# Kernel optimization log

Measured on AMD Instinct MI355X. Metric: run time of the kernel, lower is better.

Reference implementation:

```python
import jax, jax.numpy as jnp
import numpy as np

N, M, C, T, H, W = 32, 20, 512, 4, 7, 7  # batch, max_others, channels, t, h, w
L = 4  # temp_pos_len
STD = 0.01


def setup_inputs() -> dict:
    key = jax.random.key(0)
    ks = jax.random.split(key, 12)
    return {
        "person": jax.random.normal(ks[0], (N, C, T, H, W), jnp.float32),
        "others": jax.random.normal(ks[1], (N, M, C, T, H, W), jnp.float32),
        "Wq": jax.random.normal(ks[2], (C, C), jnp.float32) * STD,
        "bq": jax.random.normal(ks[3], (C,), jnp.float32) * STD,
        "Wk": jax.random.normal(ks[4], (C, C), jnp.float32) * STD,
        "bk": jax.random.normal(ks[5], (C,), jnp.float32) * STD,
        "Wv": jax.random.normal(ks[6], (C, C), jnp.float32) * STD,
        "bv": jax.random.normal(ks[7], (C,), jnp.float32) * STD,
        "Wo": jax.random.normal(ks[8], (C, C), jnp.float32) * STD,
        "bo": jax.random.normal(ks[9], (C,), jnp.float32) * STD,
        "pos_k": jax.random.normal(ks[10], (L, C), jnp.float32) * 0.02,
        "pos_v": jax.random.normal(ks[11], (L, C), jnp.float32) * 0.02,
    }


def reference(person, others, Wq, bq, Wk, bk, Wv, bv, Wo, bo, pos_k, pos_v):
    n, c, t, h, w = person.shape
    _, m, _, to, ho, wo = others.shape
    scale = c ** (-0.5)

    # 1x1x1 conv projections == channel matmuls
    q = jnp.einsum('oc,ncthw->nothw', Wq, person) + bq[None, :, None, None, None]
    k = jnp.einsum('oc,nmcthw->nmothw', Wk, others) + bk[None, None, :, None, None, None]
    v = jnp.einsum('oc,nmcthw->nmothw', Wv, others) + bv[None, None, :, None, None, None]

    # additive temporal positional bias on K/V: others split into L temporal groups
    Lp = pos_k.shape[0]
    P = m // Lp  # max_person_per_sec
    k = (k.reshape(n, Lp, P, c, to, ho, wo)
         + pos_k[None, :, None, :, None, None, None]).reshape(n, m, c, to, ho, wo)
    v = (v.reshape(n, Lp, P, c, to, ho, wo)
         + pos_v[None, :, None, :, None, None, None]).reshape(n, m, c, to, ho, wo)

    S = t * h * w          # query length
    K = m * to * ho * wo   # key length
    qf = q.reshape(n, c, S).transpose(0, 2, 1)                              # [n,S,c]
    kf = k.reshape(n, m, c, to * ho * wo).transpose(0, 1, 3, 2).reshape(n, K, c)
    vf = v.reshape(n, m, c, to * ho * wo).transpose(0, 1, 3, 2).reshape(n, K, c)

    attn = jax.nn.softmax(jnp.einsum('nsc,nkc->nsk', qf, kf) * scale, axis=-1)
    o = jnp.einsum('nsk,nkc->nsc', attn, vf)                                # [n,S,c]
    o = o.transpose(0, 2, 1).reshape(n, c, t, h, w)

    # LayerNorm over [c,t,h,w] per sample, no affine
    mu = jnp.mean(o, axis=(1, 2, 3, 4), keepdims=True)
    var = jnp.var(o, axis=(1, 2, 3, 4), keepdims=True)
    o = (o - mu) * jax.lax.rsqrt(var + 1e-5)

    o = jax.nn.relu(o)
    o = jnp.einsum('oc,ncthw->nothw', Wo, o) + bo[None, :, None, None, None]
    return o + person  # shortcut is identity (dim_person == dim_out)
```

## Files before the change

### kernel.cpp

```cpp
#include <hip/hip_runtime.h>
#include <hip/hip_bf16.h>

#define N_B 32
#define M_O 20
#define C_C 512
#define S_S 196
#define S_P 208
#define K_K 3920
#define K_P 4096
#define SCALEF 0.044194173824159216f

typedef short s4v __attribute__((ext_vector_type(4)));
typedef short s8v __attribute__((ext_vector_type(8)));
typedef float f4v __attribute__((ext_vector_type(4)));

__device__ __forceinline__ f4v mfma16(s8v a, s8v b, f4v c){
  return __builtin_amdgcn_mfma_f32_16x16x32_bf16(a, b, c, 0, 0, 0);
}
__device__ __forceinline__ unsigned short f2b(float x){
  __hip_bfloat16 h = __float2bfloat16(x);
  return *reinterpret_cast<unsigned short*>(&h);
}
__device__ __forceinline__ float b2f(short u){
  unsigned int v = ((unsigned int)(unsigned short)u) << 16;
  return __uint_as_float(v);
}

#define GLOAD16(g, l) __builtin_amdgcn_global_load_lds( \
    (const __attribute__((address_space(1))) unsigned int*)(g), \
    (__attribute__((address_space(3))) unsigned int*)(l), 16, 0, 0)

__global__ void k_sentinel(float* out, float v){ out[threadIdx.x] = v; }

__global__ void k_cvt(const float* __restrict__ w0, const float* __restrict__ w1,
                      const float* __restrict__ w2, const float* __restrict__ w3,
                      unsigned short* __restrict__ out){
  int i = blockIdx.x*256 + threadIdx.x;
  int m = i >> 16;
  int r = i & 65535;
  const float* s = (m==0)?w0:((m==1)?w1:((m==2)?w2:w3));
  f4v v = ((const f4v*)s)[r];
  s4v o = { (short)f2b(v[0]), (short)f2b(v[1]), (short)f2b(v[2]), (short)f2b(v[3]) };
  ((s4v*)out)[i] = o;
}

__global__ __launch_bounds__(256) void k_tr(const float* __restrict__ X,
                                            unsigned short* __restrict__ Xt){
  const int cc = blockIdx.x * 64;
  const int slab = blockIdx.y;
  const int tid = threadIdx.x;
  __shared__ unsigned short A[196][72];
  const int row = tid >> 2;
  const int j   = tid & 3;
  const float* src = X + (size_t)slab*(C_C*S_S) + (size_t)(cc+row)*S_S;
  for (int p = j; p < 49; p += 4){
    f4v v = *(const f4v*)(src + p*4);
    int s = p*4;
    A[s+0][row] = f2b(v[0]);
    A[s+1][row] = f2b(v[1]);
    A[s+2][row] = f2b(v[2]);
    A[s+3][row] = f2b(v[3]);
  }
  __syncthreads();
  unsigned short* dst = Xt + (size_t)slab*(S_S*C_C) + cc;
  for (int v = tid; v < S_S*8; v += 256){
    int s = v >> 3, c8 = v & 7;
    *(s8v*)(dst + (size_t)s*C_C + c8*8) = *(const s8v*)&A[s][c8*8];
  }
}

template<bool HASV>
__global__ __launch_bounds__(256, 2) void k_projgemm(
    const unsigned short* __restrict__ Xt,
    const unsigned short* __restrict__ W1, const float* __restrict__ b1, const float* __restrict__ pos1,
    const unsigned short* __restrict__ W2, const float* __restrict__ b2, const float* __restrict__ pos2,
    unsigned short* __restrict__ outK, unsigned short* __restrict__ outVT)
{
  const int id = blockIdx.x;
  const int work = HASV ? ((id & 7)*980 + (id >> 3)) : id;
  const int ct    = HASV ? (work & 3) : (work & 1);
  const int rtile = HASV ? (work >> 2) : (work >> 1);
  const int r0 = rtile*64;
  const int cb = ct * (HASV ? 128 : 256);
  const int tid = threadIdx.x, wid = tid>>6, lane = tid&63;
  const int lr = lane&15, lq = lane>>4;
  const int mat = wid >> 1, chalf = (wid & 1)*64;
  const bool isV = HASV && (mat == 1);

  const unsigned short* WB = HASV ? W2 : W1;
  const int cbB = HASV ? cb : cb + 128;

  __shared__ unsigned short SA[2][2048];
  __shared__ unsigned short SB[2][8192];

  f4v acc[4][4];
  #pragma unroll
  for (int i=0;i<4;i++)
    #pragma unroll
    for (int j=0;j<4;j++) acc[i][j]=(f4v){0,0,0,0};

  const int rsub = lane >> 2;
  const int csub = ((lane & 3) ^ ((rsub>>1)&3)) * 8;

  auto STAGE = [&](int buf, int c0){
    const unsigned short* ga = Xt + (size_t)(r0 + wid*16 + rsub)*C_C + c0 + csub;
    GLOAD16(ga, &SA[buf][(wid*16)*32]);
    #pragma unroll
    for (int j=0;j<4;j++){
      const int br = j*64 + wid*16 + rsub;
      const unsigned short* gw = (j<2)
        ? W1 + (size_t)(cb  + br      )*C_C + c0 + csub
        : WB + (size_t)(cbB + br - 128)*C_C + c0 + csub;
      GLOAD16(gw, &SB[buf][(j*64 + wid*16)*32]);
    }
  };

  STAGE(0, 0);

  const int bbase = mat*128 + chalf;
  const int rchunk = (lq ^ ((lr>>1)&3)) * 8;
  for (int it = 0; it < 16; ++it){
    const int buf = it & 1;
    if (it < 15){
      STAGE(buf^1, (it+1)*32);
      asm volatile("s_waitcnt vmcnt(5)" ::: "memory");
    } else {
      asm volatile("s_waitcnt vmcnt(0)" ::: "memory");
    }
    __builtin_amdgcn_s_barrier();
    s8v af[4], bf[4];
    #pragma unroll
    for (int i=0;i<4;i++)
      af[i] = *(const s8v*)&SA[buf][(i*16 + lr)*32 + rchunk];
    #pragma unroll
    for (int i=0;i<4;i++)
      bf[i] = *(const s8v*)&SB[buf][(bbase + i*16 + lr)*32 + rchunk];
    if (!isV){
      #pragma unroll
      for (int ot=0;ot<4;ot++)
        #pragma unroll
        for (int rt=0;rt<4;rt++)
          acc[rt][ot] = mfma16(af[rt], bf[ot], acc[rt][ot]);
    } else {
      #pragma unroll
      for (int ot=0;ot<4;ot++)
        #pragma unroll
        for (int rt=0;rt<4;rt++)
          acc[ot][rt] = mfma16(bf[ot], af[rt], acc[ot][rt]);
    }
    __builtin_amdgcn_s_barrier();
  }

  const int cout = HASV ? (cb + chalf) : (cb + mat*128 + chalf);
  if (!isV){
    #pragma unroll
    for (int ot=0;ot<4;ot++){
      const int o = cout + ot*16 + lr;
      const float bb = b1[o];
      #pragma unroll
      for (int rt=0;rt<4;rt++){
        #pragma unroll
        for (int rr=0;rr<4;rr++){
          const int r = r0 + rt*16 + lq*4 + rr;
          float bias = bb;
          if (HASV) bias += pos1[((r % K_K)/980)*C_C + o];
          outK[(size_t)r*C_C + o] = f2b(acc[rt][ot][rr] + bias);
        }
      }
    }
  } else {
    #pragma unroll
    for (int ot=0;ot<4;ot++){
      #pragma unroll
      for (int rr=0;rr<4;rr++){
        const int o = cout + ot*16 + lq*4 + rr;
        const float bb = b2[o];
        #pragma unroll
        for (int rt=0;rt<4;rt++){
          const int r = r0 + rt*16 + lr;
          const int n = r / K_K;
          const int rn = r - n*K_K;
          const float bias = bb + pos2[(rn/980)*C_C + o];
          outVT[(size_t)n*C_C*K_P + (size_t)o*K_P + rn] = f2b(acc[ot][rt][rr] + bias);
        }
      }
    }
  }
}

__global__ __launch_bounds__(512, 2) void k_scores(
    const unsigned short* __restrict__ A, const unsigned short* __restrict__ B,
    unsigned short* __restrict__ out16, float* __restrict__ rowsum)
{
  const int tid = threadIdx.x, wid = tid>>6, lane = tid&63;
  const int lr = lane&15, lq = lane>>4;
  const int wr = wid>>2, wc = wid&3;

  int x = blockIdx.x & 7, idx = blockIdx.x >> 3;
  int w = x*128 + idx;
  const int nslab = w >> 5; int sub = w & 31;
  const int ctsel = sub & 15, rtile = sub >> 4;
  const int r0 = rtile*128;
  const unsigned short* Aslab = A + (size_t)nslab*S_S*C_C;
  const unsigned short* Bslab = B + (size_t)nslab*K_K*C_C + (size_t)ctsel*256*512;

  __shared__ unsigned short SA[2][4096];
  __shared__ unsigned short SB[2][8192];

  f4v acc[4][4];
  #pragma unroll
  for (int i=0;i<4;i++)
    #pragma unroll
    for (int j=0;j<4;j++) acc[i][j]=(f4v){0,0,0,0};

  const int rsub = lane >> 2;
  const int csub = ((lane & 3) ^ ((rsub>>1)&3)) * 8;

  auto STAGE = [&](int buf, int c0){
    GLOAD16(Aslab + (size_t)(r0 + wid*16 + rsub)*512 + c0 + csub,
            &SA[buf][(wid*16)*32]);
    GLOAD16(Bslab + (size_t)(wid*16 + rsub)*512 + c0 + csub,
            &SB[buf][(wid*16)*32]);
    GLOAD16(Bslab + (size_t)(128 + wid*16 + rsub)*512 + c0 + csub,
            &SB[buf][(128 + wid*16)*32]);
  };

  STAGE(0, 0);

  const int rchunk = (lq ^ ((lr>>1)&3)) * 8;
  for (int it = 0; it < 16; ++it){
    const int buf = it & 1;
    if (it < 15){
      STAGE(buf^1, (it+1)*32);
      asm volatile("s_waitcnt vmcnt(3)" ::: "memory");
    } else {
      asm volatile("s_waitcnt vmcnt(0)" ::: "memory");
    }
    __builtin_amdgcn_s_barrier();
    s8v af[4], bf[4];
    #pragma unroll
    for (int i=0;i<4;i++)
      af[i] = *(const s8v*)&SA[buf][(wr*64 + i*16 + lr)*32 + rchunk];
    #pragma unroll
    for (int j=0;j<4;j++)
      bf[j] = *(const s8v*)&SB[buf][(wc*64 + j*16 + lr)*32 + rchunk];
    #pragma unroll
    for (int ot=0;ot<4;ot++)
      #pragma unroll
      for (int rt=0;rt<4;rt++)
        acc[rt][ot] = mfma16(af[rt], bf[ot], acc[rt][ot]);
    __builtin_amdgcn_s_barrier();
  }

  float psum[4][4];
  #pragma unroll
  for (int rt=0;rt<4;rt++)
    #pragma unroll
    for (int rr=0;rr<4;rr++) psum[rt][rr] = 0.f;

  #pragma unroll
  for (int ot=0;ot<4;ot++){
    const int kcol = ctsel*256 + wc*64 + ot*16 + lr;
    #pragma unroll
    for (int rt=0;rt<4;rt++){
      #pragma unroll
      for (int rr=0;rr<4;rr++){
        const int s = r0 + wr*64 + rt*16 + lq*4 + rr;
        float e = (kcol < K_K) ? __expf(acc[rt][ot][rr]*SCALEF) : 0.f;
        psum[rt][rr] += e;
        if (s < S_P)
          out16[((size_t)nslab*S_P + s)*K_P + kcol] = f2b(e);
      }
    }
  }
  #pragma unroll
  for (int rt=0;rt<4;rt++){
    #pragma unroll
    for (int rr=0;rr<4;rr++){
      float v = psum[rt][rr];
      v += __shfl_xor(v, 1);
      v += __shfl_xor(v, 2);
      v += __shfl_xor(v, 4);
      v += __shfl_xor(v, 8);
      if (lr == 0){
        const int s = r0 + wr*64 + rt*16 + lq*4 + rr;
        if (s < S_P) atomicAdd(&rowsum[nslab*S_P + s], v);
      }
    }
  }
}

__global__ __launch_bounds__(256, 2) void k_pv(
    const unsigned short* __restrict__ A, const unsigned short* __restrict__ B,
    const float* __restrict__ rowsum, float* __restrict__ out32)
{
  const int tid = threadIdx.x, wid = tid>>6, lane = tid&63;
  const int lr = lane&15, lq = lane>>4;
  const int wr = wid>>1, wc = wid&1;

  int x = blockIdx.x & 7, idx = blockIdx.x >> 3;
  int w = x*64 + idx;
  const int nslab = w >> 4; int sub = w & 15;
  const int ks = sub >> 3, rtile = (sub>>2)&1, ctsel = sub & 3;
  const int r0 = rtile*128;
  const int koff = ks*2048;
  const unsigned short* Aslab = A + (size_t)nslab*S_P*K_P;
  const unsigned short* Bslab = B + (size_t)nslab*C_C*K_P + (size_t)ctsel*128*K_P;

  __shared__ unsigned short SA[2][4096];
  __shared__ unsigned short SB[2][4096];

  f4v acc[4][4];
  #pragma unroll
  for (int i=0;i<4;i++)
    #pragma unroll
    for (int j=0;j<4;j++) acc[i][j]=(f4v){0,0,0,0};

  const int rsub = lane >> 2;
  const int csub = ((lane & 3) ^ ((rsub>>1)&3)) * 8;

  auto STAGE = [&](int buf, int c0){
    GLOAD16(Aslab + (size_t)(r0 + wid*16 + rsub)*K_P + c0 + csub,
            &SA[buf][(wid*16)*32]);
    GLOAD16(Aslab + (size_t)(r0 + 64 + wid*16 + rsub)*K_P + c0 + csub,
            &SA[buf][(64 + wid*16)*32]);
    GLOAD16(Bslab + (size_t)(wid*16 + rsub)*K_P + c0 + csub,
            &SB[buf][(wid*16)*32]);
    GLOAD16(Bslab + (size_t)(64 + wid*16 + rsub)*K_P + c0 + csub,
            &SB[buf][(64 + wid*16)*32]);
  };

  STAGE(0, koff);

  const int rchunk = (lq ^ ((lr>>1)&3)) * 8;
  for (int it = 0; it < 64; ++it){
    const int buf = it & 1;
    if (it < 63){
      STAGE(buf^1, koff + (it+1)*32);
      asm volatile("s_waitcnt vmcnt(4)" ::: "memory");
    } else {
      asm volatile("s_waitcnt vmcnt(0)" ::: "memory");
    }
    __builtin_amdgcn_s_barrier();
    s8v af[4], bf[4];
    #pragma unroll
    for (int i=0;i<4;i++)
      af[i] = *(const s8v*)&SA[buf][(wr*64 + i*16 + lr)*32 + rchunk];
    #pragma unroll
    for (int j=0;j<4;j++)
      bf[j] = *(const s8v*)&SB[buf][(wc*64 + j*16 + lr)*32 + rchunk];
    #pragma unroll
    for (int ot=0;ot<4;ot++)
      #pragma unroll
      for (int rt=0;rt<4;rt++)
        acc[rt][ot] = mfma16(af[rt], bf[ot], acc[rt][ot]);
    __builtin_amdgcn_s_barrier();
  }

  float invs[4][4];
  #pragma unroll
  for (int rt=0;rt<4;rt++){
    #pragma unroll
    for (int rr=0;rr<4;rr++){
      const int s = r0 + wr*64 + rt*16 + lq*4 + rr;
      invs[rt][rr] = (s < S_P) ? 1.f/rowsum[(size_t)nslab*S_P + s] : 0.f;
    }
  }
  float* op = out32 + (size_t)ks*(N_B*S_P*C_C);
  #pragma unroll
  for (int ot=0;ot<4;ot++){
    const int c = ctsel*128 + wc*64 + ot*16 + lr;
    #pragma unroll
    for (int rt=0;rt<4;rt++){
      #pragma unroll
      for (int rr=0;rr<4;rr++){
        const int s = r0 + wr*64 + rt*16 + lq*4 + rr;
        if (s < S_P)
          op[((size_t)nslab*S_P + s)*C_C + c] = acc[rt][ot][rr]*invs[rt][rr];
      }
    }
  }
}

__global__ void k_lnpart(const float* __restrict__ O0, const float* __restrict__ O1,
                         float* __restrict__ sums){
  const int part = blockIdx.x, n = blockIdx.y;
  const int tid = threadIdx.x;
  const size_t base = ((size_t)n*S_P + part*49)*C_C;
  float ls=0.f, ls2=0.f;
  for (int i = tid; i < 49*C_C/4; i += 256){
    f4v a = ((const f4v*)(O0+base))[i];
    f4v b = ((const f4v*)(O1+base))[i];
    #pragma unroll
    for (int j=0;j<4;j++){ float v = a[j]+b[j]; ls += v; ls2 += v*v; }
  }
  #pragma unroll
  for (int d=32;d>=1;d>>=1){ ls += __shfl_xor(ls,d); ls2 += __shfl_xor(ls2,d); }
  __shared__ float r1[4], r2[4];
  if ((tid&63)==0){ r1[tid>>6]=ls; r2[tid>>6]=ls2; }
  __syncthreads();
  if (tid==0){
    atomicAdd(&sums[n*2],   r1[0]+r1[1]+r1[2]+r1[3]);
    atomicAdd(&sums[n*2+1], r2[0]+r2[1]+r2[2]+r2[3]);
  }
}

__global__ void k_norm(const float* __restrict__ O0, const float* __restrict__ O1,
                       const float* __restrict__ sums, unsigned short* __restrict__ ob){
  size_t g = (size_t)blockIdx.x*256 + threadIdx.x;
  int n = (int)(g / (S_P*C_C/8));
  int rem = (int)(g - (size_t)n*(S_P*C_C/8));
  int s = rem / (C_C/8);
  const float inv = 1.f/((float)S_S*C_C);
  float mu = sums[n*2]*inv;
  float var = sums[n*2+1]*inv - mu*mu;
  float rq = rsqrtf(var + 1e-5f);
  const f4v* s0 = (const f4v*)(O0 + g*8);
  const f4v* s1 = (const f4v*)(O1 + g*8);
  f4v a0 = s0[0], a1 = s0[1], b0 = s1[0], b1 = s1[1];
  unsigned short o16[8];
  if (s < S_S){
    #pragma unroll
    for (int i=0;i<4;i++){ float y=(a0[i]+b0[i]-mu)*rq; o16[i]=f2b(fmaxf(y,0.f)); }
    #pragma unroll
    for (int i=0;i<4;i++){ float y=(a1[i]+b1[i]-mu)*rq; o16[4+i]=f2b(fmaxf(y,0.f)); }
  } else {
    #pragma unroll
    for (int i=0;i<8;i++) o16[i]=0;
  }
  *(s8v*)(ob + g*8) = *(const s8v*)o16;
}

__global__ __launch_bounds__(256) void k_final(const unsigned short* __restrict__ ob,
    const unsigned short* __restrict__ Wo, const float* __restrict__ bo,
    const float* __restrict__ person, float* __restrict__ out)
{
  const int ocb = blockIdx.x, n = blockIdx.y;
  const int tid=threadIdx.x, wid=tid>>6, lane=tid&63, lr=lane&15, lq=lane>>4;
  const int ocb0 = ocb*64 + wid*16;
  const unsigned short* obp = ob + (size_t)n*S_P*C_C;
  f4v acc[13];
  #pragma unroll
  for (int i=0;i<13;i++) acc[i]=(f4v){0,0,0,0};
  for (int c0=0;c0<C_C;c0+=32){
    s8v af = *(const s8v*)(Wo + (size_t)(ocb0+lr)*C_C + c0 + lq*8);
    #pragma unroll
    for (int ct=0;ct<13;ct++){
      s8v bfv = *(const s8v*)(obp + (size_t)(ct*16+lr)*C_C + c0 + lq*8);
      acc[ct]=mfma16(af,bfv,acc[ct]);
    }
  }
  #pragma unroll
  for (int ct=0;ct<13;ct++){
    #pragma unroll
    for (int r=0;r<4;r++){
      int oc = ocb0 + lq*4 + r;
      int s = ct*16 + lr;
      if (s < S_S){
        size_t idx = ((size_t)n*C_C + oc)*S_S + s;
        out[idx] = acc[ct][r] + bo[oc] + person[idx];
      }
    }
  }
}

extern "C" void kernel_launch(void* const* d_in, const int* in_sizes, int n_in,
                              void* d_out, int out_size, void* d_ws, size_t ws_size,
                              hipStream_t stream)
{
  (void)in_sizes; (void)n_in; (void)out_size;
  const float* person = (const float*)d_in[0];
  const float* others = (const float*)d_in[1];
  const float* Wq = (const float*)d_in[2];
  const float* bq = (const float*)d_in[3];
  const float* Wk = (const float*)d_in[4];
  const float* bk = (const float*)d_in[5];
  const float* Wv = (const float*)d_in[6];
  const float* bv = (const float*)d_in[7];
  const float* Wo = (const float*)d_in[8];
  const float* bo = (const float*)d_in[9];
  const float* pos_k = (const float*)d_in[10];
  const float* pos_v = (const float*)d_in[11];
  float* out = (float*)d_out;

  char* ws = (char*)d_ws;
  size_t off = 0;
  auto alloc = [&](size_t bytes)->char*{
    char* p = ws + off; off += (bytes + 255) & ~(size_t)255; return p;
  };
  unsigned short* Wb  = (unsigned short*)alloc(4ull*C_C*C_C*2);
  unsigned short* Xt  = (unsigned short*)alloc(((size_t)N_B*M_O*S_S + 16)*C_C*2);
  unsigned short* Qt  = (unsigned short*)alloc(((size_t)N_B*S_S + 16)*C_C*2);
  unsigned short* qb  = (unsigned short*)alloc(((size_t)N_B*S_S + 64)*C_C*2);
  unsigned short* kfb = (unsigned short*)alloc(((size_t)N_B*K_K + 256)*C_C*2);
  unsigned short* vtb = (unsigned short*)alloc((size_t)N_B*C_C*K_P*2);
  float* sums         = (float*)alloc(2*N_B*sizeof(float));
  float* rowsum       = (float*)alloc((size_t)N_B*S_P*sizeof(float));

  size_t aoff = 0;
  auto alias = [&](size_t bytes)->char*{
    char* p = (char*)Xt + aoff; aoff += (bytes + 255) & ~(size_t)255; return p;
  };
  unsigned short* Sbuf = (unsigned short*)alias(((size_t)N_B*S_P + 64)*K_P*2);
  float* Obuf          = (float*)alias(2ull*N_B*S_P*C_C*4);
  unsigned short* obb  = (unsigned short*)alias((size_t)N_B*S_P*C_C*2);

  if (off > ws_size) {
    k_sentinel<<<1,256,0,stream>>>(out, (float)(ws_size>>20));
    return;
  }

  unsigned short* Wq_b = Wb;
  unsigned short* Wk_b = Wb + 262144;
  unsigned short* Wv_b = Wb + 2*262144;
  unsigned short* Wo_b = Wb + 3*262144;
  float* O1 = Obuf + (size_t)N_B*S_P*C_C;

  hipMemsetAsync(sums, 0, 2*N_B*sizeof(float), stream);
  hipMemsetAsync(rowsum, 0, (size_t)N_B*S_P*sizeof(float), stream);
  k_cvt<<<1024,256,0,stream>>>(Wq,Wk,Wv,Wo,Wb);
  k_tr<<<dim3(8,N_B*M_O),256,0,stream>>>(others, Xt);
  k_tr<<<dim3(8,N_B),256,0,stream>>>(person, Qt);
  k_projgemm<true ><<<7840,256,0,stream>>>(Xt,
      Wk_b, bk, pos_k, Wv_b, bv, pos_v, kfb, vtb);
  k_projgemm<false><<<196,256,0,stream>>>(Qt,
      Wq_b, bq, nullptr, nullptr, nullptr, nullptr, qb, nullptr);
  k_scores<<<1024,512,0,stream>>>(qb, kfb, Sbuf, rowsum);
  k_pv<<<512,256,0,stream>>>(Sbuf, vtb, rowsum, Obuf);
  k_lnpart<<<dim3(4,N_B),256,0,stream>>>(Obuf, O1, sums);
  k_norm<<<1664,256,0,stream>>>(Obuf, O1, sums, obb);
  k_final<<<dim3(8,N_B),256,0,stream>>>(obb, Wo_b, bo, person, out);
}
```

Baseline: 581.6 us.

## Fuse fp32 transpose and bf16 conversion into projection GEMM A-tile loads

Drops the separate k_tr transpose kernels. The projection GEMM now reads the fp32 channel-major activations directly into registers, converts them to bf16 and writes them into the swizzled LDS A-tile. The loads for the next tile are issued before the MFMA work so they overlap it, and the LDS write follows the compute. This removes a full round trip of the large 'others' tensor through global memory (fp32 read, bf16 write, then re-read). In exchange the A-tile uses scalar 4-byte loads and scattered 2-byte LDS stores, which may be less efficient than the old 16-byte global_load_lds path. The attention output buffers are re-aliased onto the q/k workspace, which is no longer needed at that point.

After: 659.9 us. +13.5%, slower.

```diff
diff --git a/kernel.cpp b/kernel.cpp
--- a/kernel.cpp
+++ b/kernel.cpp
@@ -44,34 +44,9 @@
   ((s4v*)out)[i] = o;
 }
 
-__global__ __launch_bounds__(256) void k_tr(const float* __restrict__ X,
-                                            unsigned short* __restrict__ Xt){
-  const int cc = blockIdx.x * 64;
-  const int slab = blockIdx.y;
-  const int tid = threadIdx.x;
-  __shared__ unsigned short A[196][72];
-  const int row = tid >> 2;
-  const int j   = tid & 3;
-  const float* src = X + (size_t)slab*(C_C*S_S) + (size_t)(cc+row)*S_S;
-  for (int p = j; p < 49; p += 4){
-    f4v v = *(const f4v*)(src + p*4);
-    int s = p*4;
-    A[s+0][row] = f2b(v[0]);
-    A[s+1][row] = f2b(v[1]);
-    A[s+2][row] = f2b(v[2]);
-    A[s+3][row] = f2b(v[3]);
-  }
-  __syncthreads();
-  unsigned short* dst = Xt + (size_t)slab*(S_S*C_C) + cc;
-  for (int v = tid; v < S_S*8; v += 256){
-    int s = v >> 3, c8 = v & 7;
-    *(s8v*)(dst + (size_t)s*C_C + c8*8) = *(const s8v*)&A[s][c8*8];
-  }
-}
-
 template<bool HASV>
 __global__ __launch_bounds__(256, 2) void k_projgemm(
-    const unsigned short* __restrict__ Xt,
+    const float* __restrict__ X,
     const unsigned short* __restrict__ W1, const float* __restrict__ b1, const float* __restrict__ pos1,
     const unsigned short* __restrict__ W2, const float* __restrict__ b2, const float* __restrict__ pos2,
     unsigned short* __restrict__ outK, unsigned short* __restrict__ outVT)
@@ -102,9 +77,33 @@
   const int rsub = lane >> 2;
   const int csub = ((lane & 3) ^ ((rsub>>1)&3)) * 8;
 
-  auto STAGE = [&](int buf, int c0){
-    const unsigned short* ga = Xt + (size_t)(r0 + wid*16 + rsub)*C_C + c0 + csub;
-    GLOAD16(ga, &SA[buf][(wid*16)*32]);
+  const int cA = tid >> 3;
+  const int sg = tid & 7;
+  const int g0 = r0 + sg*8;
+  const int slab0 = g0 / S_S;
+  const int s0 = g0 - slab0*S_S;
+  const float* Xbase = X + (size_t)slab0*(C_C*S_S) + (size_t)cA*S_S;
+
+  float av[8];
+  auto LOADA = [&](int c0){
+    const float* bp = Xbase + (size_t)c0*S_S;
+    #pragma unroll
+    for (int j=0;j<8;j++){
+      int s = s0 + j;
+      const float* p = (s < S_S) ? (bp + s) : (bp + s + (size_t)(C_C-1)*S_S);
+      av[j] = *p;
+    }
+  };
+  auto WRITEA = [&](int buf){
+    unsigned short* sa = &SA[buf][0];
+    #pragma unroll
+    for (int j=0;j<8;j++){
+      int row = sg*8 + j;
+      int chunk = (cA >> 3) ^ ((row >> 1) & 3);
+      sa[row*32 + chunk*8 + (cA & 7)] = f2b(av[j]);
+    }
+  };
+  auto STAGEB = [&](int buf, int c0){
     #pragma unroll
     for (int j=0;j<4;j++){
       const int br = j*64 + wid*16 + rsub;
@@ -115,18 +114,23 @@
     }
   };
 
-  STAGE(0, 0);
+  LOADA(0);
+  STAGEB(0, 0);
+  asm volatile("s_waitcnt vmcnt(4)" ::: "memory");
+  WRITEA(0);
 
   const int bbase = mat*128 + chalf;
   const int rchunk = (lq ^ ((lr>>1)&3)) * 8;
   for (int it = 0; it < 16; ++it){
     const int buf = it & 1;
     if (it < 15){
-      STAGE(buf^1, (it+1)*32);
-      asm volatile("s_waitcnt vmcnt(5)" ::: "memory");
+      LOADA((it+1)*32);
+      STAGEB(buf^1, (it+1)*32);
+      asm volatile("s_waitcnt vmcnt(12)" ::: "memory");
     } else {
       asm volatile("s_waitcnt vmcnt(0)" ::: "memory");
     }
+    asm volatile("s_waitcnt lgkmcnt(0)" ::: "memory");
     __builtin_amdgcn_s_barrier();
     s8v af[4], bf[4];
     #pragma unroll
@@ -148,6 +152,11 @@
         for (int rt=0;rt<4;rt++)
           acc[ot][rt] = mfma16(bf[ot], af[rt], acc[ot][rt]);
     }
+    if (it < 15){
+      asm volatile("s_waitcnt vmcnt(4)" ::: "memory");
+      WRITEA(buf^1);
+    }
+    asm volatile("s_waitcnt lgkmcnt(0)" ::: "memory");
     __builtin_amdgcn_s_barrier();
   }
 
@@ -489,21 +498,16 @@
     char* p = ws + off; off += (bytes + 255) & ~(size_t)255; return p;
   };
   unsigned short* Wb  = (unsigned short*)alloc(4ull*C_C*C_C*2);
-  unsigned short* Xt  = (unsigned short*)alloc(((size_t)N_B*M_O*S_S + 16)*C_C*2);
-  unsigned short* Qt  = (unsigned short*)alloc(((size_t)N_B*S_S + 16)*C_C*2);
   unsigned short* qb  = (unsigned short*)alloc(((size_t)N_B*S_S + 64)*C_C*2);
   unsigned short* kfb = (unsigned short*)alloc(((size_t)N_B*K_K + 256)*C_C*2);
   unsigned short* vtb = (unsigned short*)alloc((size_t)N_B*C_C*K_P*2);
+  unsigned short* Sbuf= (unsigned short*)alloc(((size_t)N_B*S_P + 64)*K_P*2);
   float* sums         = (float*)alloc(2*N_B*sizeof(float));
   float* rowsum       = (float*)alloc((size_t)N_B*S_P*sizeof(float));
 
-  size_t aoff = 0;
-  auto alias = [&](size_t bytes)->char*{
-    char* p = (char*)Xt + aoff; aoff += (bytes + 255) & ~(size_t)255; return p;
-  };
-  unsigned short* Sbuf = (unsigned short*)alias(((size_t)N_B*S_P + 64)*K_P*2);
-  float* Obuf          = (float*)alias(2ull*N_B*S_P*C_C*4);
-  unsigned short* obb  = (unsigned short*)alias((size_t)N_B*S_P*C_C*2);
+  float* Obuf         = (float*)qb;
+  unsigned short* obb = (unsigned short*)((char*)qb +
+                          ((2ull*N_B*S_P*C_C*4 + 255) & ~(size_t)255));
 
   if (off > ws_size) {
     k_sentinel<<<1,256,0,stream>>>(out, (float)(ws_size>>20));
@@ -519,11 +523,9 @@
   hipMemsetAsync(sums, 0, 2*N_B*sizeof(float), stream);
   hipMemsetAsync(rowsum, 0, (size_t)N_B*S_P*sizeof(float), stream);
   k_cvt<<<1024,256,0,stream>>>(Wq,Wk,Wv,Wo,Wb);
-  k_tr<<<dim3(8,N_B*M_O),256,0,stream>>>(others, Xt);
-  k_tr<<<dim3(8,N_B),256,0,stream>>>(person, Qt);
-  k_projgemm<true ><<<7840,256,0,stream>>>(Xt,
+  k_projgemm<true ><<<7840,256,0,stream>>>(others,
       Wk_b, bk, pos_k, Wv_b, bv, pos_v, kfb, vtb);
-  k_projgemm<false><<<196,256,0,stream>>>(Qt,
+  k_projgemm<false><<<196,256,0,stream>>>(person,
       Wq_b, bq, nullptr, nullptr, nullptr, nullptr, qb, nullptr);
   k_scores<<<1024,512,0,stream>>>(qb, kfb, Sbuf, rowsum);
   k_pv<<<512,256,0,stream>>>(Sbuf, vtb, rowsum, Obuf);
```

## Triple-buffer LDS staging in projection, score and PV GEMM kernels

Applied to the files above, without the earlier changes.

Changes the global-to-LDS pipelines in the projection, scores and PV kernels from double to triple buffering, prefetching two k-steps ahead with matching vmcnt waits. This is meant to hide more global-load latency behind MFMA work. It also stops aliasing the score buffer onto the Xt workspace and gives it its own allocation. The larger LDS footprint per block may lower occupancy, and the workspace needs more memory.

Result: no change. 587.1 us (+0.9%).

```diff
diff --git a/kernel.cpp b/kernel.cpp
--- a/kernel.cpp
+++ b/kernel.cpp
@@ -90,8 +90,8 @@
   const unsigned short* WB = HASV ? W2 : W1;
   const int cbB = HASV ? cb : cb + 128;
 
-  __shared__ unsigned short SA[2][2048];
-  __shared__ unsigned short SB[2][8192];
+  __shared__ unsigned short SA[3][2048];
+  __shared__ unsigned short SB[3][8192];
 
   f4v acc[4][4];
   #pragma unroll
@@ -102,7 +102,8 @@
   const int rsub = lane >> 2;
   const int csub = ((lane & 3) ^ ((rsub>>1)&3)) * 8;
 
-  auto STAGE = [&](int buf, int c0){
+  auto STAGE = [&](int buf, int step){
+    const int c0 = step*32;
     const unsigned short* ga = Xt + (size_t)(r0 + wid*16 + rsub)*C_C + c0 + csub;
     GLOAD16(ga, &SA[buf][(wid*16)*32]);
     #pragma unroll
@@ -116,17 +117,16 @@
   };
 
   STAGE(0, 0);
+  STAGE(1, 1);
 
   const int bbase = mat*128 + chalf;
   const int rchunk = (lq ^ ((lr>>1)&3)) * 8;
   for (int it = 0; it < 16; ++it){
-    const int buf = it & 1;
-    if (it < 15){
-      STAGE(buf^1, (it+1)*32);
-      asm volatile("s_waitcnt vmcnt(5)" ::: "memory");
-    } else {
-      asm volatile("s_waitcnt vmcnt(0)" ::: "memory");
-    }
+    const int buf = it % 3;
+    if (it < 14) STAGE((it+2)%3, it+2);
+    if (it < 14)      asm volatile("s_waitcnt vmcnt(10)" ::: "memory");
+    else if (it < 15) asm volatile("s_waitcnt vmcnt(5)"  ::: "memory");
+    else              asm volatile("s_waitcnt vmcnt(0)"  ::: "memory");
     __builtin_amdgcn_s_barrier();
     s8v af[4], bf[4];
     #pragma unroll
@@ -204,8 +204,8 @@
   const unsigned short* Aslab = A + (size_t)nslab*S_S*C_C;
   const unsigned short* Bslab = B + (size_t)nslab*K_K*C_C + (size_t)ctsel*256*512;
 
-  __shared__ unsigned short SA[2][4096];
-  __shared__ unsigned short SB[2][8192];
+  __shared__ unsigned short SA[3][4096];
+  __shared__ unsigned short SB[3][8192];
 
   f4v acc[4][4];
   #pragma unroll
@@ -216,7 +216,8 @@
   const int rsub = lane >> 2;
   const int csub = ((lane & 3) ^ ((rsub>>1)&3)) * 8;
 
-  auto STAGE = [&](int buf, int c0){
+  auto STAGE = [&](int buf, int step){
+    const int c0 = step*32;
     GLOAD16(Aslab + (size_t)(r0 + wid*16 + rsub)*512 + c0 + csub,
             &SA[buf][(wid*16)*32]);
     GLOAD16(Bslab + (size_t)(wid*16 + rsub)*512 + c0 + csub,
@@ -226,16 +227,15 @@
   };
 
   STAGE(0, 0);
+  STAGE(1, 1);
 
   const int rchunk = (lq ^ ((lr>>1)&3)) * 8;
   for (int it = 0; it < 16; ++it){
-    const int buf = it & 1;
-    if (it < 15){
-      STAGE(buf^1, (it+1)*32);
-      asm volatile("s_waitcnt vmcnt(3)" ::: "memory");
-    } else {
-      asm volatile("s_waitcnt vmcnt(0)" ::: "memory");
-    }
+    const int buf = it % 3;
+    if (it < 14) STAGE((it+2)%3, it+2);
+    if (it < 14)      asm volatile("s_waitcnt vmcnt(6)" ::: "memory");
+    else if (it < 15) asm volatile("s_waitcnt vmcnt(3)" ::: "memory");
+    else              asm volatile("s_waitcnt vmcnt(0)" ::: "memory");
     __builtin_amdgcn_s_barrier();
     s8v af[4], bf[4];
     #pragma unroll
@@ -307,8 +307,8 @@
   const unsigned short* Aslab = A + (size_t)nslab*S_P*K_P;
   const unsigned short* Bslab = B + (size_t)nslab*C_C*K_P + (size_t)ctsel*128*K_P;
 
-  __shared__ unsigned short SA[2][4096];
-  __shared__ unsigned short SB[2][4096];
+  __shared__ unsigned short SA[3][4096];
+  __shared__ unsigned short SB[3][4096];
 
   f4v acc[4][4];
   #pragma unroll
@@ -319,7 +319,8 @@
   const int rsub = lane >> 2;
   const int csub = ((lane & 3) ^ ((rsub>>1)&3)) * 8;
 
-  auto STAGE = [&](int buf, int c0){
+  auto STAGE = [&](int buf, int step){
+    const int c0 = koff + step*32;
     GLOAD16(Aslab + (size_t)(r0 + wid*16 + rsub)*K_P + c0 + csub,
             &SA[buf][(wid*16)*32]);
     GLOAD16(Aslab + (size_t)(r0 + 64 + wid*16 + rsub)*K_P + c0 + csub,
@@ -330,17 +331,16 @@
             &SB[buf][(64 + wid*16)*32]);
   };
 
-  STAGE(0, koff);
+  STAGE(0, 0);
+  STAGE(1, 1);
 
   const int rchunk = (lq ^ ((lr>>1)&3)) * 8;
   for (int it = 0; it < 64; ++it){
-    const int buf = it & 1;
-    if (it < 63){
-      STAGE(buf^1, koff + (it+1)*32);
-      asm volatile("s_waitcnt vmcnt(4)" ::: "memory");
-    } else {
-      asm volatile("s_waitcnt vmcnt(0)" ::: "memory");
-    }
+    const int buf = it % 3;
+    if (it < 62) STAGE((it+2)%3, it+2);
+    if (it < 62)      asm volatile("s_waitcnt vmcnt(8)" ::: "memory");
+    else if (it < 63) asm volatile("s_waitcnt vmcnt(4)" ::: "memory");
+    else              asm volatile("s_waitcnt vmcnt(0)" ::: "memory");
     __builtin_amdgcn_s_barrier();
     s8v af[4], bf[4];
     #pragma unroll
@@ -494,16 +494,13 @@
   unsigned short* qb  = (unsigned short*)alloc(((size_t)N_B*S_S + 64)*C_C*2);
   unsigned short* kfb = (unsigned short*)alloc(((size_t)N_B*K_K + 256)*C_C*2);
   unsigned short* vtb = (unsigned short*)alloc((size_t)N_B*C_C*K_P*2);
+  unsigned short* Sbuf= (unsigned short*)alloc(((size_t)N_B*S_P + 64)*K_P*2);
   float* sums         = (float*)alloc(2*N_B*sizeof(float));
   float* rowsum       = (float*)alloc((size_t)N_B*S_P*sizeof(float));
 
-  size_t aoff = 0;
-  auto alias = [&](size_t bytes)->char*{
-    char* p = (char*)Xt + aoff; aoff += (bytes + 255) & ~(size_t)255; return p;
-  };
-  unsigned short* Sbuf = (unsigned short*)alias(((size_t)N_B*S_P + 64)*K_P*2);
-  float* Obuf          = (float*)alias(2ull*N_B*S_P*C_C*4);
-  unsigned short* obb  = (unsigned short*)alias((size_t)N_B*S_P*C_C*2);
+  float* Obuf         = (float*)Xt;
+  unsigned short* obb = (unsigned short*)((char*)Xt +
+                          ((2ull*N_B*S_P*C_C*4 + 255) & ~(size_t)255));
 
   if (off > ws_size) {
     k_sentinel<<<1,256,0,stream>>>(out, (float)(ws_size>>20));
```
